# Kernel tuning notes

Hardware: AMD Instinct MI355X
Metric: run time of the kernel (lower is better)

## Reference

```python
import jax, jax.numpy as jnp
import numpy as np

B, L, E = 8, 2048, 128


def setup_inputs() -> dict:
    key = jax.random.key(0)
    k1, k2, k3, k4 = jax.random.split(key, 4)
    return {
        "Uq": jax.random.normal(k1, (B, L, E), dtype=jnp.float32),
        "Uid": jax.random.normal(k2, (B, L, E), dtype=jnp.float32),
        "mask": jnp.ones((L, L), dtype=jnp.float32),
        "Wc_w": jax.random.normal(k3, (3 * E,), dtype=jnp.float32) * 0.05,
        "Wc_b": jax.random.normal(k4, (), dtype=jnp.float32) * 0.05,
    }


def reference(Uq, Uid, mask, Wc_w, Wc_b):
    # Wc(cat(Uid, Uq, Uid*Uq)) decomposed into three direct projections —
    # exact same math as the Linear over the concatenation, never
    # materializing the [B, L, L, 3E] tensor.
    e = Uq.shape[-1]
    w_id, w_q, w_mul = Wc_w[:e], Wc_w[e:2 * e], Wc_w[2 * e:]
    s_id = jnp.einsum("bie,e->bi", Uid, w_id)          # [B, Lid]
    s_q = jnp.einsum("bje,e->bj", Uq, w_q)             # [B, Lq]
    s_mul = jnp.einsum("bie,bje,e->bij", Uid, Uq, w_mul)  # [B, Lid, Lq]
    S = (s_id[:, :, None] + s_q[:, None, :] + s_mul + Wc_b) * mask
    # S_D2Q = Softmax(dim=0) over the per-example [Lid, Lq] matrix -> axis=1
    P = jax.nn.softmax(S, axis=1)                      # [B, Lid, Lq]
    A_D2Q = jnp.einsum("bij,bje->bie", P, Uq)          # [B, Lid, E]
    M = jnp.einsum("bij,bkj->bik", P, P)               # P @ P^T, [B, Lid, Lid]
    A_Q2D = jnp.einsum("bik,bke->bie", M, Uid)         # [B, Lid, E]
    Vid = jnp.concatenate([Uid, A_D2Q, Uid * A_D2Q, Uid * A_Q2D], axis=-1)
    return Vid  # [B, Lid, 4E]
```

## Files before the change

### kernel.cpp

```cpp
#include <hip/hip_runtime.h>

#define L 2048
#define E 128
#define NB 8

typedef float f32x4 __attribute__((ext_vector_type(4)));
typedef short short8 __attribute__((ext_vector_type(8)));
typedef unsigned int u32;

static __device__ inline float bf2f(ushort u) {
  union { float f; u32 i; } v; v.i = ((u32)u) << 16; return v.f;
}
static __device__ inline ushort f2bf(float f) {
  union { float f; u32 i; } v; v.f = f;
  u32 x = v.i;
  return (ushort)((x + 0x7fffu + ((x >> 16) & 1u)) >> 16);
}

__device__ inline void glds16(const ushort* g, ushort* l) {
  __builtin_amdgcn_global_load_lds(
      (const __attribute__((address_space(1))) u32*)(const void*)g,
      (__attribute__((address_space(3))) u32*)(void*)l, 16, 0, 0);
}

__global__ __launch_bounds__(512) void k_prep2(const float* __restrict__ Uq,
                                               const float* __restrict__ Uid,
                                               const float* __restrict__ Wcw,
                                               ushort* __restrict__ UqB,
                                               ushort* __restrict__ UidB,
                                               ushort* __restrict__ Uidw,
                                               ushort* __restrict__ UqT,
                                               ushort* __restrict__ UidT,
                                               float* __restrict__ s_id,
                                               float* __restrict__ s_q) {
  __shared__ float ldsW[384];
  __shared__ ushort tq[128 * 72];
  __shared__ ushort td[128 * 72];
  int t = threadIdx.x;
  if (t < 384) ldsW[t] = bf2f(f2bf(Wcw[t]));
  long r0 = (long)blockIdx.x * 64;
  int r = t >> 3;
  int e0 = (t & 7) * 16;
  __syncthreads();
  const float* pq = Uq  + (r0 + r) * E + e0;
  const float* pd = Uid + (r0 + r) * E + e0;
  float4 q4[4], d4[4];
  #pragma unroll
  for (int c = 0; c < 4; c++) { q4[c] = *(const float4*)(pq + c * 4); d4[c] = *(const float4*)(pd + c * 4); }
  ushort uqb[16], udb[16], uwb[16];
  float sid = 0.f, sq = 0.f;
  #pragma unroll
  for (int c = 0; c < 4; c++) {
    const float* qf4 = (const float*)&q4[c];
    const float* df4 = (const float*)&d4[c];
    #pragma unroll
    for (int j = 0; j < 4; j++) {
      int k = c * 4 + j;
      ushort qb = f2bf(qf4[j]), db = f2bf(df4[j]);
      float qf = bf2f(qb), df = bf2f(db);
      uqb[k] = qb; udb[k] = db;
      uwb[k] = f2bf(df * ldsW[256 + e0 + k]);
      sid += df * ldsW[e0 + k];
      sq  += qf * ldsW[128 + e0 + k];
    }
  }
  long rb = (r0 + r) * E + e0;
  *(uint4*)&UqB[rb]      = *(const uint4*)&uqb[0];
  *(uint4*)&UqB[rb + 8]  = *(const uint4*)&uqb[8];
  *(uint4*)&UidB[rb]     = *(const uint4*)&udb[0];
  *(uint4*)&UidB[rb + 8] = *(const uint4*)&udb[8];
  *(uint4*)&Uidw[rb]     = *(const uint4*)&uwb[0];
  *(uint4*)&Uidw[rb + 8] = *(const uint4*)&uwb[8];
  #pragma unroll
  for (int off = 4; off >= 1; off >>= 1) {
    sid += __shfl_xor(sid, off, 64);
    sq  += __shfl_xor(sq,  off, 64);
  }
  if ((t & 7) == 0) { s_id[r0 + r] = sid; s_q[r0 + r] = sq; }
  #pragma unroll
  for (int k = 0; k < 16; k++) {
    tq[(e0 + k) * 72 + r] = uqb[k];
    td[(e0 + k) * 72 + r] = udb[k];
  }
  __syncthreads();
  int e = t >> 2, rs = (t & 3) * 16;
  long b = r0 / L, rl = r0 - b * L;
  long ob = b * E * L + (long)e * L + rl + rs;
  uint4 v0 = *(const uint4*)&tq[e * 72 + rs];
  uint4 v1 = *(const uint4*)&tq[e * 72 + rs + 8];
  *(uint4*)&UqT[ob] = v0; *(uint4*)&UqT[ob + 8] = v1;
  v0 = *(const uint4*)&td[e * 72 + rs];
  v1 = *(const uint4*)&td[e * 72 + rs + 8];
  *(uint4*)&UidT[ob] = v0; *(uint4*)&UidT[ob + 8] = v1;
}

__global__ __launch_bounds__(256) void k_maskT(const float* __restrict__ mask,
                                               ushort* __restrict__ maskT) {
  __shared__ ushort tile[32][33];
  int j0 = blockIdx.x * 32, i0 = blockIdx.y * 32;
  int tx = threadIdx.x, ty = threadIdx.y;
  #pragma unroll
  for (int r = ty; r < 32; r += 8)
    tile[r][tx] = f2bf(mask[(long)(i0 + r) * L + j0 + tx]);
  __syncthreads();
  #pragma unroll
  for (int r = ty; r < 32; r += 8)
    maskT[(long)(j0 + r) * L + i0 + tx] = tile[tx][r];
}

__device__ inline void gemm128_loop(const ushort* __restrict__ A,
                                    const ushort* __restrict__ B,
                                    long ldA, long ldB, int K,
                                    f32x4 acc[4][4],
                                    ushort* ldsA, ushort* ldsB) {
  const int t = threadIdx.x;
  const int w = t >> 6, lane = t & 63;
  const int mrow = lane & 15, quad = lane >> 4;
  const int lr = lane >> 3;
  const int lc = ((lane & 7) ^ lr) * 8;
  const int mh = (w & 1) * 64, nh = (w >> 1) * 64;
  for (int k0 = 0; k0 < K; k0 += 64) {
    __syncthreads();
    #pragma unroll
    for (int s = 0; s < 4; s++) {
      int row = w * 32 + s * 8 + lr;
      glds16(&A[(long)row * ldA + k0 + lc], &ldsA[w * 2048 + s * 512]);
      glds16(&B[(long)row * ldB + k0 + lc], &ldsB[w * 2048 + s * 512]);
    }
    __syncthreads();
    #pragma unroll
    for (int kk = 0; kk < 2; kk++) {
      short8 av[4], bv[4];
      #pragma unroll
      for (int mi = 0; mi < 4; mi++)
        av[mi] = *(const short8*)&ldsA[(mh + mi * 16 + mrow) * 64 +
                                       ((kk * 32 + quad * 8) ^ ((mrow & 7) << 3))];
      #pragma unroll
      for (int ni = 0; ni < 4; ni++)
        bv[ni] = *(const short8*)&ldsB[(nh + ni * 16 + mrow) * 64 +
                                       ((kk * 32 + quad * 8) ^ ((mrow & 7) << 3))];
      #pragma unroll
      for (int mi = 0; mi < 4; mi++)
        #pragma unroll
        for (int ni = 0; ni < 4; ni++)
          acc[mi][ni] = __builtin_amdgcn_mfma_f32_16x16x32_bf16(av[mi], bv[ni], acc[mi][ni], 0, 0, 0);
    }
  }
}

__global__ __launch_bounds__(256) void k_scores(const ushort* __restrict__ Uq,
                                                const ushort* __restrict__ Uidw,
                                                const float* __restrict__ s_id,
                                                const float* __restrict__ s_q,
                                                const float* __restrict__ Wcb,
                                                const ushort* __restrict__ maskT,
                                                ushort* __restrict__ St,
                                                float* __restrict__ ps, int b0) {
  __shared__ ushort lds[16384];
  ushort* ldsA = lds;
  ushort* ldsB = lds + 8192;
  int bz = blockIdx.z, b = b0 + bz;
  int m0 = blockIdx.x * 128;
  int n0 = blockIdx.y * 128;
  int tile_i = blockIdx.y;
  const ushort* A = Uq   + (long)b * L * E + (long)m0 * E;
  const ushort* B = Uidw + (long)b * L * E + (long)n0 * E;
  f32x4 acc[4][4] = {};
  gemm128_loop(A, B, E, E, E, acc, ldsA, ldsB);
  float bias = bf2f(f2bf(Wcb[0]));
  const int t = threadIdx.x, w = t >> 6, lane = t & 63;
  const int col = lane & 15, quad = lane >> 4;
  const int mh = (w & 1) * 64, nh = (w >> 1) * 64;

  __syncthreads();
  float sidv[4];
  #pragma unroll
  for (int ni = 0; ni < 4; ni++)
    sidv[ni] = s_id[b * L + n0 + nh + ni * 16 + col];
  #pragma unroll
  for (int mi = 0; mi < 4; mi++) {
    float sqv[4];
    #pragma unroll
    for (int rg = 0; rg < 4; rg++)
      sqv[rg] = s_q[b * L + m0 + mh + mi * 16 + quad * 4 + rg];
    #pragma unroll
    for (int ni = 0; ni < 4; ni++) {
      int cl = nh + ni * 16 + col;
      #pragma unroll
      for (int rg = 0; rg < 4; rg++) {
        int row = mh + mi * 16 + quad * 4 + rg;
        float v = acc[mi][ni][rg] + sqv[rg] + sidv[ni] + bias;
        lds[row * 128 + (cl ^ ((row & 7) << 3))] = f2bf(v);
      }
    }
  }
  __syncthreads();
  ushort oall[64];
  #pragma unroll
  for (int p = 0; p < 8; p++) {
    int r2 = p * 16 + (t >> 4);
    int cu = (t & 15) * 8;
    uint4 sv = *(const uint4*)&lds[r2 * 128 + (cu ^ ((r2 & 7) << 3))];
    int jg = m0 + r2;
    uint4 mv = *(const uint4*)&maskT[(long)jg * L + n0 + cu];
    float lsum = 0.f;
    const ushort* sp = (const ushort*)&sv;
    const ushort* mp = (const ushort*)&mv;
    #pragma unroll
    for (int k = 0; k < 8; k++) {
      float ev = __expf(bf2f(sp[k]) * bf2f(mp[k]));
      oall[p * 8 + k] = f2bf(ev);
      lsum += bf2f(oall[p * 8 + k]);
    }
    #pragma unroll
    for (int off = 8; off >= 1; off >>= 1) lsum += __shfl_xor(lsum, off, 64);
    if ((t & 15) == 0) {
      ps[((long)bz * L + jg) * 16 + tile_i] = lsum;
    }
  }
  #pragma unroll
  for (int p = 0; p < 8; p++) {
    int r2 = p * 16 + (t >> 4);
    int cu = (t & 15) * 8;
    int jg = m0 + r2;
    *(uint4*)&St[(long)bz * L * L + (long)jg * L + n0 + cu] = *(const uint4*)&oall[p * 8];
  }
}

__global__ __launch_bounds__(256) void k_redstats(const float* __restrict__ ps,
                                                  float* __restrict__ lg) {
  int idx = blockIdx.x * 256 + threadIdx.x;
  const float* psr = ps + (long)idx * 16;
  float s = 0.f;
  #pragma unroll
  for (int k = 0; k < 16; k++) s += psr[k];
  lg[idx] = 1.0f / s;
}

__device__ inline void gemm64x64_dbuf(const ushort* __restrict__ A,
                                      const ushort* __restrict__ B,
                                      long ldA, long ldB, int K,
                                      f32x4 acc[2][2],
                                      ushort* ldsA, ushort* ldsB) {
  const int t = threadIdx.x;
  const int w = t >> 6, lane = t & 63;
  const int mrow = lane & 15, quad = lane >> 4;
  const int lr = lane >> 3;
  const int lc = ((lane & 7) ^ lr) * 8;
  const int mh = (w & 1) * 32, nh = (w >> 1) * 32;
  #pragma unroll
  for (int s = 0; s < 2; s++) {
    int row = w * 16 + s * 8 + lr;
    glds16(&A[(long)row * ldA + lc], &ldsA[w * 1024 + s * 512]);
    glds16(&B[(long)row * ldB + lc], &ldsB[w * 1024 + s * 512]);
  }
  int cur = 0;
  for (int k0 = 0; k0 < K; k0 += 64) {
    __syncthreads();
    int nxt = cur ^ 1;
    if (k0 + 64 < K) {
      #pragma unroll
      for (int s = 0; s < 2; s++) {
        int row = w * 16 + s * 8 + lr;
        glds16(&A[(long)row * ldA + k0 + 64 + lc], &ldsA[nxt * 4096 + w * 1024 + s * 512]);
        glds16(&B[(long)row * ldB + k0 + 64 + lc], &ldsB[nxt * 4096 + w * 1024 + s * 512]);
      }
    }
    const ushort* cA = &ldsA[cur * 4096];
    const ushort* cB = &ldsB[cur * 4096];
    #pragma unroll
    for (int kk = 0; kk < 2; kk++) {
      short8 av[2], bv[2];
      #pragma unroll
      for (int mi = 0; mi < 2; mi++)
        av[mi] = *(const short8*)&cA[(mh + mi * 16 + mrow) * 64 +
                                     ((kk * 32 + quad * 8) ^ ((mrow & 7) << 3))];
      #pragma unroll
      for (int ni = 0; ni < 2; ni++)
        bv[ni] = *(const short8*)&cB[(nh + ni * 16 + mrow) * 64 +
                                     ((kk * 32 + quad * 8) ^ ((mrow & 7) << 3))];
      #pragma unroll
      for (int mi = 0; mi < 2; mi++)
        #pragma unroll
        for (int ni = 0; ni < 2; ni++)
          acc[mi][ni] = __builtin_amdgcn_mfma_f32_16x16x32_bf16(av[mi], bv[ni], acc[mi][ni], 0, 0, 0);
    }
    cur = nxt;
  }
}

__global__ __launch_bounds__(256) void k_gemm_Tt(const ushort* __restrict__ UidT,
                                                 const ushort* __restrict__ Et,
                                                 const float* __restrict__ lg,
                                                 ushort* __restrict__ Tt, int b0) {
  __shared__ ushort lds[16384];
  ushort* ldsA = lds;
  ushort* ldsB = lds + 8192;
  int bz = blockIdx.z, b = b0 + bz;
  int e0 = (blockIdx.x & 1) * 64;
  int j0 = (blockIdx.x >> 1) * 64;
  const ushort* A = UidT + (long)b * E * L + (long)e0 * L;
  const ushort* B = Et   + (long)bz * L * L + (long)j0 * L;
  f32x4 acc[2][2] = {};
  gemm64x64_dbuf(A, B, L, L, L, acc, ldsA, ldsB);
  const int t = threadIdx.x, w = t >> 6, lane = t & 63;
  const int col = lane & 15, quad = lane >> 4;
  const int mh = (w & 1) * 32, nh = (w >> 1) * 32;
  __syncthreads();
  #pragma unroll
  for (int mi = 0; mi < 2; mi++)
    #pragma unroll
    for (int ni = 0; ni < 2; ni++) {
      int cl = nh + ni * 16 + col;
      float sc = lg[(long)bz * L + j0 + cl];
      #pragma unroll
      for (int rg = 0; rg < 4; rg++) {
        int row = mh + mi * 16 + quad * 4 + rg;
        lds[row * 64 + (cl ^ ((row & 7) << 3))] = f2bf(acc[mi][ni][rg] * sc);
      }
    }
  __syncthreads();
  #pragma unroll
  for (int p = 0; p < 2; p++) {
    int r2 = p * 32 + (t >> 3);
    int cu = (t & 7) * 8;
    uint4 v = *(const uint4*)&lds[r2 * 64 + (cu ^ ((r2 & 7) << 3))];
    *(uint4*)&Tt[(long)b * E * L + (long)(e0 + r2) * L + j0 + cu] = v;
  }
}

__global__ __launch_bounds__(512) void k_gemm_A(const ushort* __restrict__ Et,
                                                const ushort* __restrict__ UqT,
                                                const ushort* __restrict__ Tt,
                                                const ushort* __restrict__ UidB,
                                                const float* __restrict__ lg,
                                                float* __restrict__ out, int b0) {
  __shared__ ushort ldsA[2 * 4608];
  __shared__ ushort ldsB[2 * 8192];
  int bz = blockIdx.z, b = b0 + bz;
  int m0 = blockIdx.x * 64;
  int n0 = blockIdx.y * 128;
  const ushort* Eb = Et + (long)bz * L * L + m0;
  const float* lgb = lg + (long)bz * L;
  const ushort* B = (blockIdx.y == 0) ? (UqT + (long)b * E * L)
                                      : (Tt  + (long)b * E * L);
  const int t = threadIdx.x, w = t >> 6, lane = t & 63;
  const int mrow = lane & 15, quad = lane >> 4;
  const int lr = lane >> 3;
  const int lc = ((lane & 7) ^ lr) * 8;
  const int mh = (w & 1) * 32, nh = (w >> 1) * 32;
  const int jp2 = (t >> 4) * 2;
  const int ic  = (t & 15) * 4;
  f32x4 acc[2][2] = {};
  uint2 q0 = *(const uint2*)&Eb[(long)jp2 * L + ic];
  uint2 q1 = *(const uint2*)&Eb[(long)(jp2 + 1) * L + ic];
  float s0 = lgb[jp2], s1 = lgb[jp2 + 1];
  #pragma unroll
  for (int s = 0; s < 2; s++) {
    int row = w * 16 + s * 8 + lr;
    glds16(&B[(long)row * L + lc], &ldsB[w * 1024 + s * 512]);
  }
  {
    const ushort* p0 = (const ushort*)&q0;
    const ushort* p1 = (const ushort*)&q1;
    #pragma unroll
    for (int k = 0; k < 4; k++) {
      u32 pk = (u32)f2bf(bf2f(p0[k]) * s0) |
               ((u32)f2bf(bf2f(p1[k]) * s1) << 16);
      int i = ic + k;
      int cs = jp2 ^ (((i >> 3) & 7) << 3);
      *(u32*)&ldsA[i * 72 + cs] = pk;
    }
  }
  q0 = *(const uint2*)&Eb[(long)(64 + jp2) * L + ic];
  q1 = *(const uint2*)&Eb[(long)(64 + jp2 + 1) * L + ic];
  s0 = lgb[64 + jp2]; s1 = lgb[64 + jp2 + 1];

  int cur = 0;
  for (int k0 = 0; k0 < L; k0 += 64) {
    __syncthreads();
    int nxt = cur ^ 1;
    if (k0 + 64 < L) {
      #pragma unroll
      for (int s = 0; s < 2; s++) {
        int row = w * 16 + s * 8 + lr;
        glds16(&B[(long)row * L + k0 + 64 + lc], &ldsB[nxt * 8192 + w * 1024 + s * 512]);
      }
      const ushort* p0 = (const ushort*)&q0;
      const ushort* p1 = (const ushort*)&q1;
      #pragma unroll
      for (int k = 0; k < 4; k++) {
        u32 pk = (u32)f2bf(bf2f(p0[k]) * s0) |
                 ((u32)f2bf(bf2f(p1[k]) * s1) << 16);
        int i = ic + k;
        int cs = jp2 ^ (((i >> 3) & 7) << 3);
        *(u32*)&ldsA[nxt * 4608 + i * 72 + cs] = pk;
      }
    }
    if (k0 + 128 < L) {
      q0 = *(const uint2*)&Eb[(long)(k0 + 128 + jp2) * L + ic];
      q1 = *(const uint2*)&Eb[(long)(k0 + 128 + jp2 + 1) * L + ic];
      s0 = lgb[k0 + 128 + jp2]; s1 = lgb[k0 + 128 + jp2 + 1];
    }
    const ushort* cA = &ldsA[cur * 4608];
    const ushort* cB = &ldsB[cur * 8192];
    #pragma unroll
    for (int kk = 0; kk < 2; kk++) {
      short8 av[2], bv[2];
      #pragma unroll
      for (int mi = 0; mi < 2; mi++) {
        int i = mh + mi * 16 + mrow;
        av[mi] = *(const short8*)&cA[i * 72 +
                   ((kk * 32 + quad * 8) ^ (((i >> 3) & 7) << 3))];
      }
      #pragma unroll
      for (int ni = 0; ni < 2; ni++)
        bv[ni] = *(const short8*)&cB[(nh + ni * 16 + mrow) * 64 +
                                     ((kk * 32 + quad * 8) ^ ((mrow & 7) << 3))];
      #pragma unroll
      for (int mi = 0; mi < 2; mi++)
        #pragma unroll
        for (int ni = 0; ni < 2; ni++)
          acc[mi][ni] = __builtin_amdgcn_mfma_f32_16x16x32_bf16(av[mi], bv[ni], acc[mi][ni], 0, 0, 0);
    }
    cur = nxt;
  }
  const int col = mrow;
  #pragma unroll
  for (int mi = 0; mi < 2; mi++)
    #pragma unroll
    for (int ni = 0; ni < 2; ni++)
      #pragma unroll
      for (int rg = 0; rg < 4; rg++) {
        int ig = m0 + mh + mi * 16 + quad * 4 + rg;
        int c  = n0 + nh + ni * 16 + col;
        float a = acc[mi][ni][rg];
        float uidf = bf2f(UidB[(long)b * L * E + (long)ig * E + (c & 127)]);
        long ob = ((long)b * L + ig) * 512;
        if (c < 128) {
          out[ob + c]       = uidf;
          out[ob + 128 + c] = a;
          out[ob + 256 + c] = uidf * a;
        } else {
          out[ob + 256 + c] = uidf * a;
        }
      }
}

extern "C" void kernel_launch(void* const* d_in, const int* in_sizes, int n_in,
                              void* d_out, int out_size, void* d_ws, size_t ws_size,
                              hipStream_t stream) {
  const float* Uq   = (const float*)d_in[0];
  const float* Uid  = (const float*)d_in[1];
  const float* mask = (const float*)d_in[2];
  const float* Wcw  = (const float*)d_in[3];
  const float* Wcb  = (const float*)d_in[4];
  float* out = (float*)d_out;

  char* ws = (char*)d_ws;
  size_t off = 0;
  auto alloc = [&](size_t bytes) -> void* {
    void* p = ws + off; off += (bytes + 255) & ~(size_t)255; return p;
  };
  const size_t nUb = (size_t)NB * L * E * 2;
  ushort* UqB   = (ushort*)alloc(nUb);
  ushort* UidB  = (ushort*)alloc(nUb);
  ushort* Uidw  = (ushort*)alloc(nUb);
  ushort* UqT   = (ushort*)alloc(nUb);
  ushort* UidT  = (ushort*)alloc(nUb);
  ushort* Tt    = (ushort*)alloc(nUb);
  ushort* maskT = (ushort*)alloc((size_t)L * L * 2);
  float*  s_id  = (float*)alloc((size_t)NB * L * 4);
  float*  s_q   = (float*)alloc((size_t)NB * L * 4);
  float*  lg    = (float*)alloc((size_t)NB * L * 4);
  float*  ps    = (float*)alloc((size_t)NB * L * 16 * 4);
  const size_t per_batch = (size_t)L * L * 2;
  size_t avail = (ws_size > off + per_batch) ? (ws_size - off) : per_batch;
  int nb_c = (int)(avail / per_batch);
  if (nb_c < 1) nb_c = 1;
  if (nb_c > NB) nb_c = NB;
  ushort* St = (ushort*)(ws + off);

  dim3 tb(32, 8);
  k_prep2<<<NB * L / 64, 512, 0, stream>>>(Uq, Uid, Wcw, UqB, UidB, Uidw, UqT, UidT, s_id, s_q);
  k_maskT<<<dim3(L / 32, L / 32), tb, 0, stream>>>(mask, maskT);

  for (int b0 = 0; b0 < NB; b0 += nb_c) {
    int nb = (NB - b0 < nb_c) ? (NB - b0) : nb_c;
    k_scores<<<dim3(L / 128, L / 128, nb), 256, 0, stream>>>(UqB, Uidw, s_id, s_q, Wcb, maskT, St, ps, b0);
    k_redstats<<<dim3(nb * L / 256), 256, 0, stream>>>(ps, lg);
    k_gemm_Tt<<<dim3(2 * (L / 64), 1, nb), 256, 0, stream>>>(UidT, St, lg, Tt, b0);
    k_gemm_A<<<dim3(L / 64, 2, nb), 512, 0, stream>>>(St, UqT, Tt, UidB, lg, out, b0);
  }
}
```

Baseline: 197.8 us.

## Move softmax normalization from P operand onto Uq and squared Tt scale

```diff
diff --git a/kernel.cpp b/kernel.cpp
--- a/kernel.cpp
+++ b/kernel.cpp
@@ -210,7 +210,7 @@
     for (int k = 0; k < 8; k++) {
       float ev = __expf(bf2f(sp[k]) * bf2f(mp[k]));
       oall[p * 8 + k] = f2bf(ev);
-      lsum += bf2f(oall[p * 8 + k]);
+      lsum += ev;
     }
     #pragma unroll
     for (int off = 8; off >= 1; off >>= 1) lsum += __shfl_xor(lsum, off, 64);
@@ -235,6 +235,20 @@
   #pragma unroll
   for (int k = 0; k < 16; k++) s += psr[k];
   lg[idx] = 1.0f / s;
+}
+
+__global__ __launch_bounds__(256) void k_scaleUq(const ushort* __restrict__ UqT,
+                                                 const float* __restrict__ lg,
+                                                 ushort* __restrict__ UqS, int b0) {
+  int bz = blockIdx.y, b = b0 + bz;
+  long base = (long)blockIdx.x * 2048 + threadIdx.x * 8;
+  int j = (int)(base & (L - 1));
+  uint4 v = *(const uint4*)&UqT[(long)b * E * L + base];
+  const ushort* p = (const ushort*)&v;
+  ushort o[8];
+  #pragma unroll
+  for (int k = 0; k < 8; k++) o[k] = f2bf(bf2f(p[k]) * lg[bz * L + j + k]);
+  *(uint4*)&UqS[(long)b * E * L + base] = *(const uint4*)&o[0];
 }
 
 __device__ inline void gemm64x64_dbuf(const ushort* __restrict__ A,
@@ -312,7 +326,8 @@
     #pragma unroll
     for (int ni = 0; ni < 2; ni++) {
       int cl = nh + ni * 16 + col;
-      float sc = lg[(long)bz * L + j0 + cl];
+      float scv = lg[(long)bz * L + j0 + cl];
+      float sc = scv * scv;
       #pragma unroll
       for (int rg = 0; rg < 4; rg++) {
         int row = mh + mi * 16 + quad * 4 + rg;
@@ -330,10 +345,9 @@
 }
 
 __global__ __launch_bounds__(512) void k_gemm_A(const ushort* __restrict__ Et,
-                                                const ushort* __restrict__ UqT,
+                                                const ushort* __restrict__ UqS,
                                                 const ushort* __restrict__ Tt,
                                                 const ushort* __restrict__ UidB,
-                                                const float* __restrict__ lg,
                                                 float* __restrict__ out, int b0) {
   __shared__ ushort ldsA[2 * 4608];
   __shared__ ushort ldsB[2 * 8192];
@@ -341,8 +355,7 @@
   int m0 = blockIdx.x * 64;
   int n0 = blockIdx.y * 128;
   const ushort* Eb = Et + (long)bz * L * L + m0;
-  const float* lgb = lg + (long)bz * L;
-  const ushort* B = (blockIdx.y == 0) ? (UqT + (long)b * E * L)
+  const ushort* B = (blockIdx.y == 0) ? (UqS + (long)b * E * L)
                                       : (Tt  + (long)b * E * L);
   const int t = threadIdx.x, w = t >> 6, lane = t & 63;
   const int mrow = lane & 15, quad = lane >> 4;
@@ -354,7 +367,6 @@
   f32x4 acc[2][2] = {};
   uint2 q0 = *(const uint2*)&Eb[(long)jp2 * L + ic];
   uint2 q1 = *(const uint2*)&Eb[(long)(jp2 + 1) * L + ic];
-  float s0 = lgb[jp2], s1 = lgb[jp2 + 1];
   #pragma unroll
   for (int s = 0; s < 2; s++) {
     int row = w * 16 + s * 8 + lr;
@@ -365,8 +377,7 @@
     const ushort* p1 = (const ushort*)&q1;
     #pragma unroll
     for (int k = 0; k < 4; k++) {
-      u32 pk = (u32)f2bf(bf2f(p0[k]) * s0) |
-               ((u32)f2bf(bf2f(p1[k]) * s1) << 16);
+      u32 pk = (u32)p0[k] | ((u32)p1[k] << 16);
       int i = ic + k;
       int cs = jp2 ^ (((i >> 3) & 7) << 3);
       *(u32*)&ldsA[i * 72 + cs] = pk;
@@ -374,7 +385,6 @@
   }
   q0 = *(const uint2*)&Eb[(long)(64 + jp2) * L + ic];
   q1 = *(const uint2*)&Eb[(long)(64 + jp2 + 1) * L + ic];
-  s0 = lgb[64 + jp2]; s1 = lgb[64 + jp2 + 1];
 
   int cur = 0;
   for (int k0 = 0; k0 < L; k0 += 64) {
@@ -390,8 +400,7 @@
       const ushort* p1 = (const ushort*)&q1;
       #pragma unroll
       for (int k = 0; k < 4; k++) {
-        u32 pk = (u32)f2bf(bf2f(p0[k]) * s0) |
-                 ((u32)f2bf(bf2f(p1[k]) * s1) << 16);
+        u32 pk = (u32)p0[k] | ((u32)p1[k] << 16);
         int i = ic + k;
         int cs = jp2 ^ (((i >> 3) & 7) << 3);
         *(u32*)&ldsA[nxt * 4608 + i * 72 + cs] = pk;
@@ -400,7 +409,6 @@
     if (k0 + 128 < L) {
       q0 = *(const uint2*)&Eb[(long)(k0 + 128 + jp2) * L + ic];
       q1 = *(const uint2*)&Eb[(long)(k0 + 128 + jp2 + 1) * L + ic];
-      s0 = lgb[k0 + 128 + jp2]; s1 = lgb[k0 + 128 + jp2 + 1];
     }
     const ushort* cA = &ldsA[cur * 4608];
     const ushort* cB = &ldsB[cur * 8192];
@@ -468,6 +476,7 @@
   ushort* Uidw  = (ushort*)alloc(nUb);
   ushort* UqT   = (ushort*)alloc(nUb);
   ushort* UidT  = (ushort*)alloc(nUb);
+  ushort* UqS   = (ushort*)alloc(nUb);
   ushort* Tt    = (ushort*)alloc(nUb);
   ushort* maskT = (ushort*)alloc((size_t)L * L * 2);
   float*  s_id  = (float*)alloc((size_t)NB * L * 4);
@@ -489,7 +498,8 @@
     int nb = (NB - b0 < nb_c) ? (NB - b0) : nb_c;
     k_scores<<<dim3(L / 128, L / 128, nb), 256, 0, stream>>>(UqB, Uidw, s_id, s_q, Wcb, maskT, St, ps, b0);
     k_redstats<<<dim3(nb * L / 256), 256, 0, stream>>>(ps, lg);
+    k_scaleUq<<<dim3(E * L / 2048, nb), 256, 0, stream>>>(UqT, lg, UqS, b0);
     k_gemm_Tt<<<dim3(2 * (L / 64), 1, nb), 256, 0, stream>>>(UidT, St, lg, Tt, b0);
-    k_gemm_A<<<dim3(L / 64, 2, nb), 512, 0, stream>>>(St, UqT, Tt, UidB, lg, out, b0);
-  }
-}
+    k_gemm_A<<<dim3(L / 64, 2, nb), 512, 0, stream>>>(St, UqS, Tt, UidB, out, b0);
+  }
+}
```

New measurement: 196.0 us. Within noise of the previous version (-0.9%).
